# Optimization experiments

Measured on AMD Instinct MI355X. Metric: run time of the kernel, lower is better.

Reference implementation:

```python
import jax, jax.numpy as jnp
import numpy as np

B, N, C, F, OUT = 4, 512, 1024, 1024, 1024
LOC = 128  # min(128, out_channels)
EPS_BN = 1e-5


def _batchnorm(x, g, b):
    # BatchNorm1d in training mode: biased batch stats over rows
    m = jnp.mean(x, axis=0)
    v = jnp.var(x, axis=0)
    return (x - m) / jnp.sqrt(v + EPS_BN) * g + b


def _relative_pe(loc):
    # loc: [N,4] (x,y,w,h) -> [N,N,LOC]; faithfully replicates the torch
    # cat([N,4N]) -> view(-1,4) interleaving of the original code.
    cx = loc[:, 0] + 0.5 * loc[:, 2]
    cy = loc[:, 1] + 0.5 * loc[:, 3]
    w, h = loc[:, 2], loc[:, 3]
    eps = jnp.float32(1e-3)
    dx = jnp.maximum(jnp.abs(cx[:, None] - cx[None, :]) / w[None, :], eps)
    dy = jnp.maximum(jnp.abs(cy[:, None] - cy[None, :]) / h[None, :], eps)
    dw = w[:, None] / w[None, :]
    dh = h[:, None] / h[None, :]
    delta = jnp.log(jnp.concatenate([dx, dy, dw, dh], axis=-1))  # [N,4N]
    delta = delta.reshape(-1, 4)                                  # [N*N,4]
    d = LOC // 8
    pe = jnp.exp(2.0 * jnp.arange(d, dtype=jnp.float32) / d * np.log(1000.0))
    ang = delta[:, :, None] / pe                                  # [N*N,4,d]
    emb = jnp.concatenate([jnp.sin(ang), jnp.cos(ang)], axis=-1)  # [N*N,4,2d]
    return emb.reshape(N, N, LOC)


def reference(box_features, boxes, bn1_g, bn1_b, Wq, bq, Wk, bk, Wv, bv, Wr, br, bn2_g, bn2_b):
    feat = _batchnorm(box_features, bn1_g, bn1_b).reshape(B, N, C)

    def per_image(f, loc):
        rel = jnp.squeeze(_relative_pe(loc) @ Wr + br, axis=-1)   # [N,N]
        q = f @ Wq + bq
        k = f @ Wk + bk
        v = f @ Wv + bv
        att = q @ k.T / jnp.sqrt(jnp.float32(F)) + jax.nn.log_softmax(rel, axis=-1)
        return jax.nn.softmax(att, axis=-1) @ v                   # [N,OUT]

    out = jax.vmap(per_image)(feat, boxes).reshape(B * N, OUT)
    return _batchnorm(out, bn2_g, bn2_b)


def setup_inputs() -> dict:
    key = jax.random.key(0)
    ks = jax.random.split(key, 10)
    box_features = jax.random.normal(ks[0], (B * N, C), dtype=jnp.float32)
    u = jax.random.uniform(ks[1], (B, N, 4), dtype=jnp.float32)
    xy = u[..., :2] * 800.0
    wh = 16.0 + u[..., 2:] * 240.0
    boxes = jnp.concatenate([xy, wh], axis=-1)
    s = 0.02
    return {
        "box_features": box_features,
        "boxes": boxes,
        "bn1_g": jnp.ones((C,), jnp.float32),
        "bn1_b": jnp.zeros((C,), jnp.float32),
        "Wq": jax.random.normal(ks[2], (C, F), jnp.float32) * s,
        "bq": jnp.zeros((F,), jnp.float32),
        "Wk": jax.random.normal(ks[3], (C, F), jnp.float32) * s,
        "bk": jnp.zeros((F,), jnp.float32),
        "Wv": jax.random.normal(ks[4], (C, OUT), jnp.float32) * s,
        "bv": jnp.zeros((OUT,), jnp.float32),
        "Wr": jax.random.normal(ks[5], (LOC, 1), jnp.float32) * s,
        "br": jnp.zeros((1,), jnp.float32),
        "bn2_g": jnp.ones((OUT,), jnp.float32),
        "bn2_b": jnp.zeros((OUT,), jnp.float32),
    }
```

## Files before the change

kernel.cpp:

```cpp
#include <hip/hip_runtime.h>
#include <math.h>

typedef __bf16 bf16;
typedef __attribute__((ext_vector_type(8))) __bf16 bf16x8;
typedef __attribute__((ext_vector_type(4))) __bf16 bf16x4;
typedef __attribute__((ext_vector_type(4))) float f32x4;

#define NCH1 128
#define RPC1 16

#define XD0   (-6.93f)
#define XSPAN (11.03f)
#define XINVH (1023.f / 11.03f)

__global__ __launch_bounds__(256)
void prep(const float* __restrict__ Wq, const float* __restrict__ Wk, const float* __restrict__ Wv,
          bf16* __restrict__ T0, bf16* __restrict__ T1, bf16* __restrict__ T2,
          const float* __restrict__ bq, const float* __restrict__ bk, float* __restrict__ biasqk,
          const float* __restrict__ X, float* __restrict__ psum, float* __restrict__ psq,
          const float* __restrict__ boxes, const float* __restrict__ Wr, const float* __restrict__ br,
          float* __restrict__ ent, float* __restrict__ tabs)
{
    __shared__ float tile[64][65];
    const int bid = blockIdx.x;
    const int tid = threadIdx.x;

    if (bid < 768) {
        const int mat = bid >> 8, g2 = bid & 255;
        const float* W = (mat == 0) ? Wq : (mat == 1) ? Wk : Wv;
        bf16* T        = (mat == 0) ? T0 : (mat == 1) ? T1 : T2;
        const int bx = (g2 & 15) * 64, by = (g2 >> 4) * 64;
        const int tx = tid & 63, ty = tid >> 6;
#pragma unroll
        for (int i = 0; i < 16; ++i)
            tile[ty + i * 4][tx] = W[(long)(by + ty + i * 4) * 1024 + bx + tx];
        __syncthreads();
#pragma unroll
        for (int i = 0; i < 16; ++i)
            T[(long)(bx + ty + i * 4) * 1024 + by + tx] = (bf16)tile[tx][ty + i * 4];
    } else if (bid < 896) {
        const int c4 = tid;
        const long r0 = (long)(bid - 768) * RPC1;
        const float4* Xv = (const float4*)X;
        float4 s = {0.f,0.f,0.f,0.f}, q = {0.f,0.f,0.f,0.f};
#pragma unroll
        for (int r = 0; r < RPC1; ++r) {
            float4 x = Xv[(r0 + r) * 256 + c4];
            s.x += x.x; s.y += x.y; s.z += x.z; s.w += x.w;
            q.x += x.x*x.x; q.y += x.y*x.y; q.z += x.z*x.z; q.w += x.w*x.w;
        }
        ((float4*)psum)[(bid - 768) * 256 + c4] = s;
        ((float4*)psq) [(bid - 768) * 256 + c4] = q;
    } else if (bid == 896) {
        for (int e = tid; e < 2048; e += 256) {
            float4 b4 = ((const float4*)boxes)[e];
            float w = b4.z, h = b4.w;
            ent[0*2048+e] = b4.x + 0.5f * w;
            ent[1*2048+e] = b4.y + 0.5f * h;
            ent[2*2048+e] = __logf(w);
            ent[3*2048+e] = __logf(h);
            ent[4*2048+e] = 1e-3f * w;
            ent[5*2048+e] = 1e-3f * h;
        }
        for (int i = tid; i < 2048; i += 256)
            biasqk[i] = (i < 1024) ? bq[i] : bk[i - 1024];
    } else {
        const int c = bid - 897;
        float* tb = tabs + c * 1024;
        const float brq = 0.25f * br[0];
        const float hstep = XSPAN / 1023.f;
        for (int e = tid; e < 1024; e += 256) {
            float d = XD0 + hstep * (float)e;
            float a = brq;
#pragma unroll
            for (int k = 0; k < 16; ++k) {
                float tk = exp2f(-1.24572303558f * (float)k);
                float s_, c_;
                __sincosf(d * tk, &s_, &c_);
                a += s_ * Wr[c * 32 + k] + c_ * Wr[c * 32 + 16 + k];
            }
            tb[e] = a;
        }
    }
}

template <int NCH_, int BF16OUT>
__global__ __launch_bounds__(256)
void bn_final_apply(const float* __restrict__ X, const float* __restrict__ psum,
                    const float* __restrict__ psq, const float* __restrict__ g,
                    const float* __restrict__ b, void* __restrict__ Yp)
{
    __shared__ float ls[4][64], lq[4][64], ssc[64], ssh[64];
    const int t  = threadIdx.x;
    const int cs = blockIdx.x;
    const int rc = blockIdx.y;
    const int col_l = t & 63, part = t >> 6;
    const int col = cs * 64 + col_l;
    constexpr int CPT = NCH_ / 4;
    float s = 0.f, q = 0.f;
#pragma unroll
    for (int i = 0; i < CPT; ++i) {
        int ch = part * CPT + i;
        s += psum[ch * 1024 + col];
        q += psq [ch * 1024 + col];
    }
    ls[part][col_l] = s; lq[part][col_l] = q;
    __syncthreads();
    if (t < 64) {
        float S = ls[0][t]+ls[1][t]+ls[2][t]+ls[3][t];
        float Q = lq[0][t]+lq[1][t]+lq[2][t]+lq[3][t];
        float m = S / 2048.f;
        float v = Q / 2048.f - m*m;
        float inv = 1.0f / sqrtf(v + 1e-5f);
        float sc = g[cs*64+t] * inv;
        ssc[t] = sc; ssh[t] = b[cs*64+t] - m*sc;
    }
    __syncthreads();
    const int f = t & 15, rsub = t >> 4;
    float4 sc4 = ((const float4*)ssc)[f];
    float4 sh4 = ((const float4*)ssh)[f];
#pragma unroll
    for (int it = 0; it < 8; ++it) {
        int row = rc*128 + it*16 + rsub;
        float4 x = ((const float4*)(X + (long)row*1024 + cs*64))[f];
        float4 rv;
        rv.x = x.x*sc4.x + sh4.x;
        rv.y = x.y*sc4.y + sh4.y;
        rv.z = x.z*sc4.z + sh4.z;
        rv.w = x.w*sc4.w + sh4.w;
        if constexpr (BF16OUT) {
            bf16x4 y;
            y[0]=(bf16)rv.x; y[1]=(bf16)rv.y; y[2]=(bf16)rv.z; y[3]=(bf16)rv.w;
            ((bf16x4*)((bf16*)Yp + (long)row*1024 + cs*64))[f] = y;
        } else {
            ((float4*)((float*)Yp + (long)row*1024 + cs*64))[f] = rv;
        }
    }
}

__device__ __forceinline__ float look(const float* tab, float d)
{
    float t = (d - XD0) * XINVH;
    t = fminf(fmaxf(t, 0.f), 1022.999f);
    float fi = floorf(t);
    int i = (int)fi;
    float a = tab[i], b = tab[i + 1];
    return a + (b - a) * (t - fi);
}

__device__ __forceinline__ void stage_tile_128x32(const bf16* __restrict__ src_base, int ld,
                                                  int row0, int k0, bf16* lds_base, int w, int l)
{
#pragma unroll
    for (int t = 0; t < 2; ++t) {
        int rchunk = w * 32 + t * 16;
        const bf16* src = src_base + (long)(row0 + rchunk + (l >> 2)) * ld + k0 + (l & 3) * 8;
        __builtin_amdgcn_global_load_lds((__attribute__((address_space(1))) void*)src,
                                         (__attribute__((address_space(3))) void*)(lds_base + rchunk * 32),
                                         16, 0, 0);
    }
}

template <int MODE>
__device__ __forceinline__ void gemm_body(
    const bf16* __restrict__ Ab, int lda, const bf16* __restrict__ Bb, int ldb,
    void* __restrict__ Cp, int ldc, int K, int bm, int bn,
    const float* __restrict__ bias, char* smem)
{
    bf16* As0 = (bf16*)smem;
    bf16* Bs0 = (bf16*)(smem + 16384);
    const int tid = threadIdx.x;
    const int w = tid >> 6, l = tid & 63;
    const int wr = w >> 1, wc = w & 1;

    f32x4 acc[4][4];
#pragma unroll
    for (int i = 0; i < 4; ++i)
#pragma unroll
        for (int j = 0; j < 4; ++j) acc[i][j] = (f32x4){0.f,0.f,0.f,0.f};

    const int nkt = K >> 5;
    stage_tile_128x32(Ab, lda, bm, 0, As0, w, l);
    stage_tile_128x32(Bb, ldb, bn, 0, Bs0, w, l);
    __syncthreads();

    const int fr = l & 15;
    const int ko = (l >> 4) * 8;

    for (int kt = 0; kt < nkt; ++kt) {
        const int cur = kt & 1;
        bf16* Asc = As0 + cur * 4096;
        bf16* Bsc = Bs0 + cur * 4096;
        if (kt + 1 < nkt) {
            stage_tile_128x32(Ab, lda, bm, (kt + 1) << 5, As0 + (cur ^ 1) * 4096, w, l);
            stage_tile_128x32(Bb, ldb, bn, (kt + 1) << 5, Bs0 + (cur ^ 1) * 4096, w, l);
        }
        bf16x8 af[4], bfv[4];
#pragma unroll
        for (int mi = 0; mi < 4; ++mi)
            af[mi] = *(const bf16x8*)(&Asc[(wr * 64 + mi * 16 + fr) * 32 + ko]);
#pragma unroll
        for (int ni = 0; ni < 4; ++ni)
            bfv[ni] = *(const bf16x8*)(&Bsc[(wc * 64 + ni * 16 + fr) * 32 + ko]);
#pragma unroll
        for (int mi = 0; mi < 4; ++mi)
#pragma unroll
            for (int ni = 0; ni < 4; ++ni)
                acc[mi][ni] = __builtin_amdgcn_mfma_f32_16x16x32_bf16(af[mi], bfv[ni], acc[mi][ni], 0, 0, 0);
        __syncthreads();
    }

    const int crow0 = bm + wr * 64 + (l >> 4) * 4;
    const int ccol0 = bn + wc * 64 + fr;
#pragma unroll
    for (int mi = 0; mi < 4; ++mi)
#pragma unroll
        for (int ni = 0; ni < 4; ++ni)
#pragma unroll
            for (int r = 0; r < 4; ++r) {
                const int row = crow0 + mi * 16 + r;
                const int col = ccol0 + ni * 16;
                const float v = acc[mi][ni][r];
                if constexpr (MODE == 0) {
                    ((bf16*)Cp)[(long)row * ldc + col] = (bf16)(v + bias[col]);
                } else {
                    ((bf16*)Cp)[(long)row * ldc + col] = (bf16)(v + bias[row]);
                }
            }
}

__global__ __launch_bounds__(256, 2)
void megaGEMM(const bf16* __restrict__ featbf, const bf16* __restrict__ WqkT,
              const bf16* __restrict__ WvT, bf16* __restrict__ qkbf, bf16* __restrict__ vTbf,
              const float* __restrict__ biasqk, const float* __restrict__ bv)
{
    __shared__ char smem[32768];
    const unsigned bid = blockIdx.x;
    const unsigned g = bid / 3u, r = bid % 3u;
    if (r < 2) {
        const unsigned t = g * 2 + r;
        gemm_body<0>(featbf, 1024, WqkT, 1024, qkbf, 2048, 1024, (t & 15) * 128, (t >> 4) * 128,
                     biasqk, smem);
    } else {
        const int img = g >> 5, rem = g & 31;
        gemm_body<1>(WvT, 1024, featbf + (long)img * 524288, 1024,
                     vTbf + (long)img * 524288, 512, 1024, (rem >> 2) * 128, (rem & 3) * 128,
                     bv, smem);
    }
}

__device__ __forceinline__ void stage64(const bf16* __restrict__ src_base, int ld,
                                        int row0, int k0, bf16* lds_base, int w, int l)
{
    const bf16* src = src_base + (long)(row0 + w * 16 + (l >> 2)) * ld + k0 + (l & 3) * 8;
    __builtin_amdgcn_global_load_lds((__attribute__((address_space(1))) void*)src,
                                     (__attribute__((address_space(3))) void*)(lds_base + w * 16 * 32),
                                     16, 0, 0);
}

__global__ __launch_bounds__(256, 4)
void attn64(const bf16* __restrict__ qk, float* __restrict__ S0, float* __restrict__ S1,
            const float* __restrict__ ent, const float* __restrict__ tabs)
{
    __shared__ char smem[20480];
    const int img = blockIdx.z >> 1, kh = blockIdx.z & 1;
    const int bm = blockIdx.x * 64, bn = blockIdx.y * 64;
    const bf16* A = qk + (long)img * 1048576 + kh * 512;
    const bf16* B = qk + 1024 + (long)img * 1048576 + kh * 512;
    bf16* As0 = (bf16*)smem;
    bf16* Bs0 = (bf16*)(smem + 8192);

    const int tid = threadIdx.x;
    const int w = tid >> 6, l = tid & 63;
    const int wr = w >> 1, wc = w & 1;
    const int fr = l & 15;
    const int ko = (l >> 4) * 8;

    f32x4 acc[2][2];
#pragma unroll
    for (int i = 0; i < 2; ++i)
#pragma unroll
        for (int j = 0; j < 2; ++j) acc[i][j] = (f32x4){0.f,0.f,0.f,0.f};

    stage64(A, 2048, bm, 0, As0, w, l);
    stage64(B, 2048, bn, 0, Bs0, w, l);
    __syncthreads();

    for (int kt = 0; kt < 16; ++kt) {
        const int cur = kt & 1;
        bf16* Asc = As0 + cur * 2048;
        bf16* Bsc = Bs0 + cur * 2048;
        if (kt + 1 < 16) {
            stage64(A, 2048, bm, (kt + 1) << 5, As0 + (cur ^ 1) * 2048, w, l);
            stage64(B, 2048, bn, (kt + 1) << 5, Bs0 + (cur ^ 1) * 2048, w, l);
        }
        bf16x8 af[2], bfv[2];
#pragma unroll
        for (int mi = 0; mi < 2; ++mi)
            af[mi] = *(const bf16x8*)(&Asc[(wr * 32 + mi * 16 + fr) * 32 + ko]);
#pragma unroll
        for (int ni = 0; ni < 2; ++ni)
            bfv[ni] = *(const bf16x8*)(&Bsc[(wc * 32 + ni * 16 + fr) * 32 + ko]);
#pragma unroll
        for (int mi = 0; mi < 2; ++mi)
#pragma unroll
            for (int ni = 0; ni < 2; ++ni)
                acc[mi][ni] = __builtin_amdgcn_mfma_f32_16x16x32_bf16(af[mi], bfv[ni], acc[mi][ni], 0, 0, 0);
        __syncthreads();
    }

    const float scale = 0.03125f;
    float* Sout = (kh == 0 ? S0 : S1) + (long)img * 262144;

    if (kh == 1) {
#pragma unroll
        for (int mi = 0; mi < 2; ++mi)
#pragma unroll
            for (int ni = 0; ni < 2; ++ni)
#pragma unroll
                for (int r = 0; r < 4; ++r) {
                    const int rowl = wr * 32 + mi * 16 + (l >> 4) * 4 + r;
                    const int coll = wc * 32 + ni * 16 + fr;
                    Sout[(long)(bm + rowl) * 512 + bn + coll] = acc[mi][ni][r] * scale;
                }
        return;
    }

    float* stab = (float*)smem;
    float* RA   = stab + 4096;
    float* SA   = RA + 64;
    float* SE   = SA + 260;
    float* SL   = SE + 260;
    const int b   = bn >> 7;
    const int jj0 = (bn & 64) * 4;
    for (int i = tid; i < 4096; i += 256) stab[i] = tabs[i];
    {
        const int eb = img * 512;
        if (tid < 64) RA[tid] = ent[b * 2048 + eb + bm + tid];
        for (int u = tid; u < 260 && jj0 + u < 512; u += 256) {
            SA[u] = ent[b * 2048 + eb + jj0 + u];
            if (b < 2) {
                SE[u] = ent[(4 + b) * 2048 + eb + jj0 + u];
                SL[u] = ent[(2 + b) * 2048 + eb + jj0 + u];
            }
        }
    }
    __syncthreads();
#pragma unroll
    for (int ni = 0; ni < 2; ++ni) {
        const int coll = wc * 32 + ni * 16 + fr;
        const int u0   = 4 * coll;
        const float sA0 = SA[u0], sA1 = SA[u0+1], sA2 = SA[u0+2], sA3 = SA[u0+3];
        float sE0=0.f,sE1=0.f,sE2=0.f,sE3=0.f, sL0=0.f,sL1=0.f,sL2=0.f,sL3=0.f;
        if (b < 2) {
            sE0 = SE[u0]; sE1 = SE[u0+1]; sE2 = SE[u0+2]; sE3 = SE[u0+3];
            sL0 = SL[u0]; sL1 = SL[u0+1]; sL2 = SL[u0+2]; sL3 = SL[u0+3];
        }
#pragma unroll
        for (int mi = 0; mi < 2; ++mi)
#pragma unroll
            for (int r = 0; r < 4; ++r) {
                const int rowl = wr * 32 + mi * 16 + (l >> 4) * 4 + r;
                const float ai = RA[rowl];
                float d0, d1, d2, d3;
                if (b < 2) {
                    d0 = __logf(fmaxf(fabsf(ai - sA0), sE0)) - sL0;
                    d1 = __logf(fmaxf(fabsf(ai - sA1), sE1)) - sL1;
                    d2 = __logf(fmaxf(fabsf(ai - sA2), sE2)) - sL2;
                    d3 = __logf(fmaxf(fabsf(ai - sA3), sE3)) - sL3;
                } else {
                    d0 = ai - sA0; d1 = ai - sA1; d2 = ai - sA2; d3 = ai - sA3;
                }
                float relv = look(stab,        d0) + look(stab + 1024, d1)
                           + look(stab + 2048, d2) + look(stab + 3072, d3);
                Sout[(long)(bm + rowl) * 512 + bn + coll] = acc[mi][ni][r] * scale + relv;
            }
    }
}

__global__ __launch_bounds__(256)
void softmax2(const float* __restrict__ S0, const float* __restrict__ S1, bf16* __restrict__ P)
{
    const long row = blockIdx.x;
    const int t = threadIdx.x;
    float x0 = S0[row * 512 + t]       + S1[row * 512 + t];
    float x1 = S0[row * 512 + t + 256] + S1[row * 512 + t + 256];
    float mx = fmaxf(x0, x1);
#pragma unroll
    for (int off = 32; off; off >>= 1) mx = fmaxf(mx, __shfl_xor(mx, off));
    __shared__ float redm[4], reds[4];
    if ((t & 63) == 0) redm[t >> 6] = mx;
    __syncthreads();
    mx = fmaxf(fmaxf(redm[0], redm[1]), fmaxf(redm[2], redm[3]));
    float e0 = __expf(x0 - mx), e1 = __expf(x1 - mx);
    float sm = e0 + e1;
#pragma unroll
    for (int off = 32; off; off >>= 1) sm += __shfl_xor(sm, off);
    if ((t & 63) == 0) reds[t >> 6] = sm;
    __syncthreads();
    sm = (reds[0] + reds[1]) + (reds[2] + reds[3]);
    float inv = 1.0f / sm;
    P[row * 512 + t]       = (bf16)(e0 * inv);
    P[row * 512 + t + 256] = (bf16)(e1 * inv);
}

__global__ __launch_bounds__(256, 4)
void pv64(const bf16* __restrict__ P, const bf16* __restrict__ vT, float* __restrict__ out,
          float* __restrict__ psum, float* __restrict__ psq)
{
    __shared__ char smem[16384];
    const int img = blockIdx.z;
    const int bm = blockIdx.x * 64, bn = blockIdx.y * 64;
    const bf16* A = P  + (long)img * 262144;
    const bf16* B = vT + (long)img * 524288;
    float* C = out + (long)img * 524288;
    bf16* As0 = (bf16*)smem;
    bf16* Bs0 = (bf16*)(smem + 8192);

    const int tid = threadIdx.x;
    const int w = tid >> 6, l = tid & 63;
    const int wr = w >> 1, wc = w & 1;
    const int fr = l & 15;
    const int ko = (l >> 4) * 8;

    f32x4 acc[2][2];
#pragma unroll
    for (int i = 0; i < 2; ++i)
#pragma unroll
        for (int j = 0; j < 2; ++j) acc[i][j] = (f32x4){0.f,0.f,0.f,0.f};

    stage64(A, 512, bm, 0, As0, w, l);
    stage64(B, 512, bn, 0, Bs0, w, l);
    __syncthreads();

    for (int kt = 0; kt < 16; ++kt) {
        const int cur = kt & 1;
        bf16* Asc = As0 + cur * 2048;
        bf16* Bsc = Bs0 + cur * 2048;
        if (kt + 1 < 16) {
            stage64(A, 512, bm, (kt + 1) << 5, As0 + (cur ^ 1) * 2048, w, l);
            stage64(B, 512, bn, (kt + 1) << 5, Bs0 + (cur ^ 1) * 2048, w, l);
        }
        bf16x8 af[2], bfv[2];
#pragma unroll
        for (int mi = 0; mi < 2; ++mi)
            af[mi] = *(const bf16x8*)(&Asc[(wr * 32 + mi * 16 + fr) * 32 + ko]);
#pragma unroll
        for (int ni = 0; ni < 2; ++ni)
            bfv[ni] = *(const bf16x8*)(&Bsc[(wc * 32 + ni * 16 + fr) * 32 + ko]);
#pragma unroll
        for (int mi = 0; mi < 2; ++mi)
#pragma unroll
            for (int ni = 0; ni < 2; ++ni)
                acc[mi][ni] = __builtin_amdgcn_mfma_f32_16x16x32_bf16(af[mi], bfv[ni], acc[mi][ni], 0, 0, 0);
        __syncthreads();
    }

#pragma unroll
    for (int mi = 0; mi < 2; ++mi)
#pragma unroll
        for (int ni = 0; ni < 2; ++ni)
#pragma unroll
            for (int r = 0; r < 4; ++r) {
                const int rowl = wr * 32 + mi * 16 + (l >> 4) * 4 + r;
                const int coll = wc * 32 + ni * 16 + fr;
                C[(long)(bm + rowl) * 1024 + bn + coll] = acc[mi][ni][r];
            }

    float s_[2], q_[2];
#pragma unroll
    for (int ni = 0; ni < 2; ++ni) {
        float s = 0.f, q = 0.f;
#pragma unroll
        for (int mi = 0; mi < 2; ++mi)
#pragma unroll
            for (int r = 0; r < 4; ++r) { float v = acc[mi][ni][r]; s += v; q += v * v; }
        s_[ni] = s; q_[ni] = q;
    }
#pragma unroll
    for (int ni = 0; ni < 2; ++ni) {
        s_[ni] += __shfl_xor(s_[ni], 16); s_[ni] += __shfl_xor(s_[ni], 32);
        q_[ni] += __shfl_xor(q_[ni], 16); q_[ni] += __shfl_xor(q_[ni], 32);
    }
    float* lred = (float*)smem;
    __syncthreads();
    if (l < 16) {
#pragma unroll
        for (int ni = 0; ni < 2; ++ni) {
            const int c = wc * 32 + ni * 16 + l;
            lred[(wr * 2 + 0) * 64 + c] = s_[ni];
            lred[(wr * 2 + 1) * 64 + c] = q_[ni];
        }
    }
    __syncthreads();
    if (tid < 64) {
        const int chunk = img * 8 + blockIdx.x;
        psum[chunk * 1024 + bn + tid] = lred[0 * 64 + tid] + lred[2 * 64 + tid];
        psq [chunk * 1024 + bn + tid] = lred[1 * 64 + tid] + lred[3 * 64 + tid];
    }
}

extern "C" void kernel_launch(void* const* d_in, const int* in_sizes, int n_in,
                              void* d_out, int out_size, void* d_ws, size_t ws_size,
                              hipStream_t stream)
{
    const float* box_features = (const float*)d_in[0];
    const float* boxes  = (const float*)d_in[1];
    const float* bn1_g  = (const float*)d_in[2];
    const float* bn1_b  = (const float*)d_in[3];
    const float* Wq     = (const float*)d_in[4];
    const float* bq     = (const float*)d_in[5];
    const float* Wk     = (const float*)d_in[6];
    const float* bk     = (const float*)d_in[7];
    const float* Wv     = (const float*)d_in[8];
    const float* bv     = (const float*)d_in[9];
    const float* Wr     = (const float*)d_in[10];
    const float* br     = (const float*)d_in[11];
    const float* bn2_g  = (const float*)d_in[12];
    const float* bn2_b  = (const float*)d_in[13];
    float* out = (float*)d_out;

    char* ws = (char*)d_ws;
    const long MB = 1024 * 1024;
    float* psum   = (float*)(ws + 0);
    float* psq    = (float*)(ws + 512 * 1024);
    float* biasqk = (float*)(ws + 1 * MB);
    float* ent    = (float*)(ws + 1 * MB + 65536);
    float* tabs   = (float*)(ws + 1 * MB + 131072);
    bf16*  featbf = (bf16*)(ws + 2 * MB);
    bf16*  WqkT   = (bf16*)(ws + 6 * MB);
    float* Sbuf1  = (float*)(ws + 6 * MB);
    bf16*  WvT    = (bf16*)(ws + 10 * MB);
    bf16*  qkbf   = (bf16*)(ws + 12 * MB);
    bf16*  vTbf   = (bf16*)(ws + 20 * MB);
    float* Sbuf0  = (float*)(ws + 24 * MB);
    bf16*  Pbuf   = (bf16*)(ws + 28 * MB);

    prep<<<dim3(901, 1, 1), dim3(256, 1, 1), 0, stream>>>(
        Wq, Wk, Wv, WqkT, WqkT + 1024 * 1024, WvT, bq, bk, biasqk,
        box_features, psum, psq, boxes, Wr, br, ent, tabs);

    bn_final_apply<NCH1, 1><<<dim3(16, 16, 1), dim3(256, 1, 1), 0, stream>>>(
        box_features, psum, psq, bn1_g, bn1_b, featbf);

    megaGEMM<<<dim3(384, 1, 1), dim3(256, 1, 1), 0, stream>>>(
        featbf, WqkT, WvT, qkbf, vTbf, biasqk, bv);

    attn64<<<dim3(8, 8, 8), dim3(256, 1, 1), 0, stream>>>(qkbf, Sbuf0, Sbuf1, ent, tabs);

    softmax2<<<dim3(2048, 1, 1), dim3(256, 1, 1), 0, stream>>>(Sbuf0, Sbuf1, Pbuf);

    pv64<<<dim3(8, 16, 4), dim3(256, 1, 1), 0, stream>>>(Pbuf, vTbf, out, psum, psq);

    bn_final_apply<32, 0><<<dim3(16, 16, 1), dim3(256, 1, 1), 0, stream>>>(
        out, psum, psq, bn2_g, bn2_b, out);
}
```

Baseline: 87.95 us.

## Move V projection GEMM from QK launch into attention-score launch

The QK projection now runs alone as a 256-block GEMM. The V^T projection GEMM blocks are interleaved into the attention-score kernel: one GEMM tile for every four attention tiles, 640 blocks in total. This rebalances the two launches so the V projection overlaps with score computation instead of lengthening the first GEMM launch. The trade-off is that the attention tiles now run with the GEMM's larger shared-memory footprint and a lower launch-bounds occupancy hint (2 instead of 4).

```diff
diff --git a/kernel.cpp b/kernel.cpp
--- a/kernel.cpp
+++ b/kernel.cpp
@@ -161,10 +161,19 @@
     }
 }
 
+__device__ __forceinline__ void stage64(const bf16* __restrict__ src_base, int ld,
+                                        int row0, int k0, bf16* lds_base, int w, int l)
+{
+    const bf16* src = src_base + (long)(row0 + w * 16 + (l >> 2)) * ld + k0 + (l & 3) * 8;
+    __builtin_amdgcn_global_load_lds((__attribute__((address_space(1))) void*)src,
+                                     (__attribute__((address_space(3))) void*)(lds_base + w * 16 * 32),
+                                     16, 0, 0);
+}
+
 template <int MODE>
 __device__ __forceinline__ void gemm_body(
     const bf16* __restrict__ Ab, int lda, const bf16* __restrict__ Bb, int ldb,
-    void* __restrict__ Cp, int ldc, int K, int bm, int bn,
+    bf16* __restrict__ Cp, int ldc, int K, int bm, int bn,
     const float* __restrict__ bias, char* smem)
 {
     bf16* As0 = (bf16*)smem;
@@ -222,49 +231,30 @@
                 const int col = ccol0 + ni * 16;
                 const float v = acc[mi][ni][r];
                 if constexpr (MODE == 0) {
-                    ((bf16*)Cp)[(long)row * ldc + col] = (bf16)(v + bias[col]);
+                    Cp[(long)row * ldc + col] = (bf16)(v + bias[col]);
                 } else {
-                    ((bf16*)Cp)[(long)row * ldc + col] = (bf16)(v + bias[row]);
+                    Cp[(long)row * ldc + col] = (bf16)(v + bias[row]);
                 }
             }
 }
 
 __global__ __launch_bounds__(256, 2)
-void megaGEMM(const bf16* __restrict__ featbf, const bf16* __restrict__ WqkT,
-              const bf16* __restrict__ WvT, bf16* __restrict__ qkbf, bf16* __restrict__ vTbf,
-              const float* __restrict__ biasqk, const float* __restrict__ bv)
+void qkGEMM(const bf16* __restrict__ featbf, const bf16* __restrict__ WqkT,
+            bf16* __restrict__ qkbf, const float* __restrict__ biasqk)
 {
     __shared__ char smem[32768];
-    const unsigned bid = blockIdx.x;
-    const unsigned g = bid / 3u, r = bid % 3u;
-    if (r < 2) {
-        const unsigned t = g * 2 + r;
-        gemm_body<0>(featbf, 1024, WqkT, 1024, qkbf, 2048, 1024, (t & 15) * 128, (t >> 4) * 128,
-                     biasqk, smem);
-    } else {
-        const int img = g >> 5, rem = g & 31;
-        gemm_body<1>(WvT, 1024, featbf + (long)img * 524288, 1024,
-                     vTbf + (long)img * 524288, 512, 1024, (rem >> 2) * 128, (rem & 3) * 128,
-                     bv, smem);
-    }
-}
-
-__device__ __forceinline__ void stage64(const bf16* __restrict__ src_base, int ld,
-                                        int row0, int k0, bf16* lds_base, int w, int l)
-{
-    const bf16* src = src_base + (long)(row0 + w * 16 + (l >> 2)) * ld + k0 + (l & 3) * 8;
-    __builtin_amdgcn_global_load_lds((__attribute__((address_space(1))) void*)src,
-                                     (__attribute__((address_space(3))) void*)(lds_base + w * 16 * 32),
-                                     16, 0, 0);
-}
-
-__global__ __launch_bounds__(256, 4)
-void attn64(const bf16* __restrict__ qk, float* __restrict__ S0, float* __restrict__ S1,
-            const float* __restrict__ ent, const float* __restrict__ tabs)
-{
-    __shared__ char smem[20480];
-    const int img = blockIdx.z >> 1, kh = blockIdx.z & 1;
-    const int bm = blockIdx.x * 64, bn = blockIdx.y * 64;
+    const unsigned t = blockIdx.x;
+    gemm_body<0>(featbf, 1024, WqkT, 1024, qkbf, 2048, 1024,
+                 (t & 15) * 128, (t >> 4) * 128, biasqk, smem);
+}
+
+__device__ __forceinline__ void attn_body(
+    const bf16* __restrict__ qk, float* __restrict__ S0, float* __restrict__ S1,
+    const float* __restrict__ ent, const float* __restrict__ tabs,
+    int bx, int by, int bz, char* smem)
+{
+    const int img = bz >> 1, kh = bz & 1;
+    const int bm = bx * 64, bn = by * 64;
     const bf16* A = qk + (long)img * 1048576 + kh * 512;
     const bf16* B = qk + 1024 + (long)img * 1048576 + kh * 512;
     bf16* As0 = (bf16*)smem;
@@ -378,6 +368,26 @@
     }
 }
 
+__global__ __launch_bounds__(256, 2)
+void attn_vt(const bf16* __restrict__ qk, float* __restrict__ S0, float* __restrict__ S1,
+             const float* __restrict__ ent, const float* __restrict__ tabs,
+             const bf16* __restrict__ featbf, const bf16* __restrict__ WvT,
+             bf16* __restrict__ vTbf, const float* __restrict__ bv)
+{
+    __shared__ char smem[32768];
+    const unsigned bid = blockIdx.x;
+    const unsigned g = bid / 5u, r = bid % 5u;
+    if (r < 4) {
+        const unsigned idx = g * 4 + r;
+        attn_body(qk, S0, S1, ent, tabs, idx & 7, (idx >> 3) & 7, idx >> 6, smem);
+    } else {
+        const int img = g >> 5, rem = g & 31;
+        gemm_body<1>(WvT, 1024, featbf + (long)img * 524288, 1024,
+                     vTbf + (long)img * 524288, 512, 1024,
+                     (rem >> 2) * 128, (rem & 3) * 128, bv, smem);
+    }
+}
+
 __global__ __launch_bounds__(256)
 void softmax2(const float* __restrict__ S0, const float* __restrict__ S1, bf16* __restrict__ P)
 {
@@ -543,10 +553,10 @@
     bn_final_apply<NCH1, 1><<<dim3(16, 16, 1), dim3(256, 1, 1), 0, stream>>>(
         box_features, psum, psq, bn1_g, bn1_b, featbf);
 
-    megaGEMM<<<dim3(384, 1, 1), dim3(256, 1, 1), 0, stream>>>(
-        featbf, WqkT, WvT, qkbf, vTbf, biasqk, bv);
-
-    attn64<<<dim3(8, 8, 8), dim3(256, 1, 1), 0, stream>>>(qkbf, Sbuf0, Sbuf1, ent, tabs);
+    qkGEMM<<<dim3(256, 1, 1), dim3(256, 1, 1), 0, stream>>>(featbf, WqkT, qkbf, biasqk);
+
+    attn_vt<<<dim3(640, 1, 1), dim3(256, 1, 1), 0, stream>>>(
+        qkbf, Sbuf0, Sbuf1, ent, tabs, featbf, WvT, vTbf, bv);
 
     softmax2<<<dim3(2048, 1, 1), dim3(256, 1, 1), 0, stream>>>(Sbuf0, Sbuf1, Pbuf);
 
```

Result: slower. 90.17 us (+2.5%).
